# Kernel optimization log

Hardware: AMD Instinct MI355X
Metric: run time of the kernel (lower is better)

## Reference

```python
import jax, jax.numpy as jnp
import numpy as np

EPS = 1e-5


def setup_inputs() -> dict:
    key = jax.random.key(0)
    k1, k2, k3, k4, k5 = jax.random.split(key, 5)
    N, d, F = 8192, 768, 32768
    return {
        "x": jax.random.normal(k1, (N, d), dtype=jnp.float32),
        "pre_bias": jax.random.normal(k2, (d,), dtype=jnp.float32) * 0.02,
        "latent_bias": jax.random.normal(k3, (F,), dtype=jnp.float32) * 0.02,
        "enc_w": jax.random.normal(k4, (F, d), dtype=jnp.float32) / np.sqrt(d),
        "dec_w": jax.random.normal(k5, (d, F), dtype=jnp.float32) / np.sqrt(F),
        "k": 32,
    }


def reference(x, pre_bias, latent_bias, enc_w, dec_w, k):
    # --- encode: manual layernorm (keep mean/std for de-norm) ---
    mean = jnp.mean(x, axis=-1, keepdims=True)           # (N,1)
    var = jnp.var(x, axis=-1, keepdims=True)             # unbiased=False
    std = jnp.sqrt(var + EPS)
    x_centered = (x - mean) / std - pre_bias             # (N,d)
    h_pre = x_centered @ enc_w.T + latent_bias           # (N,F)
    # --- top-k ReLU: keep k largest pre-activations, relu them ---
    topk_vals, topk_idx = jax.lax.top_k(h_pre, k)        # (N,k)
    h = jnp.put_along_axis(jnp.zeros_like(h_pre), topk_idx,
                           jax.nn.relu(topk_vals), axis=-1, inplace=False)
    # --- decode + de-normalize ---
    x_rec_norm = h @ dec_w.T + pre_bias                  # (N,d)
    x_hat = x_rec_norm * std + mean
    return x_hat
```

## Files before the change

### kernel.cpp

```cpp
#include <hip/hip_runtime.h>
#include <hip/hip_bf16.h>
#include <stdint.h>

#define N_ROWS 8192
#define DIM 768
#define NF 32768
#define TOPK 32
#define CANDCAP 72
#define RTHRESH 44

typedef __attribute__((ext_vector_type(8))) short bf16x8;
typedef __attribute__((ext_vector_type(8))) short short8;
typedef __attribute__((ext_vector_type(4))) float f32x4;

__device__ inline void async_ld16(const void* g, void* l) {
  __builtin_amdgcn_global_load_lds(
      (const __attribute__((address_space(1))) unsigned int*)g,
      (__attribute__((address_space(3))) unsigned int*)l, 16, 0, 0);
}

__device__ inline unsigned short f2bf(float f) {
  union { float f; unsigned u; } c; c.f = f;
  unsigned r = c.u + 0x7FFFu + ((c.u >> 16) & 1u);
  return (unsigned short)(r >> 16);
}

__device__ inline float bf2f(unsigned short u) {
  union { unsigned u; float f; } c; c.u = ((unsigned)u) << 16;
  return c.f;
}

__device__ inline void block_barrier_fenced() {
  __builtin_amdgcn_s_barrier();
  asm volatile("" ::: "memory");
  __builtin_amdgcn_sched_barrier(0);
}

__global__ __launch_bounds__(256) void k_ln(const float* __restrict__ x,
                                            const float* __restrict__ pre_bias,
                                            unsigned short* __restrict__ xh,
                                            float* __restrict__ meanA,
                                            float* __restrict__ stdA) {
  int row = blockIdx.x;
  int tid = threadIdx.x;
  int lane = tid & 63, wv = tid >> 6;
  const float* xr = x + (size_t)row * DIM;
  float a0 = xr[tid], a1 = xr[tid + 256], a2 = xr[tid + 512];
  __shared__ float red[8];
  float s = a0 + a1 + a2;
  for (int off = 32; off > 0; off >>= 1) s += __shfl_down(s, off);
  if (lane == 0) red[wv] = s;
  __syncthreads();
  float mean;
  if (tid == 0) { mean = (red[0] + red[1] + red[2] + red[3]) / (float)DIM; red[4] = mean; }
  __syncthreads();
  mean = red[4];
  float d0 = a0 - mean, d1 = a1 - mean, d2 = a2 - mean;
  float ss = d0 * d0 + d1 * d1 + d2 * d2;
  for (int off = 32; off > 0; off >>= 1) ss += __shfl_down(ss, off);
  if (lane == 0) red[wv] = ss;
  __syncthreads();
  float stdv;
  if (tid == 0) {
    float var = (red[0] + red[1] + red[2] + red[3]) / (float)DIM;
    stdv = sqrtf(var + 1e-5f);
    red[5] = stdv;
    meanA[row] = mean;
    stdA[row] = stdv;
  }
  __syncthreads();
  stdv = red[5];
  float inv = 1.0f / stdv;
  unsigned short* xo = xh + (size_t)row * DIM;
  xo[tid]       = f2bf(d0 * inv - pre_bias[tid]);
  xo[tid + 256] = f2bf(d1 * inv - pre_bias[tid + 256]);
  xo[tid + 512] = f2bf(d2 * inv - pre_bias[tid + 512]);
}

__global__ __launch_bounds__(256) void k_cv(const float* __restrict__ w,
                                            unsigned short* __restrict__ o, int n4) {
  int i = blockIdx.x * 256 + threadIdx.x;
  if (i >= n4) return;
  float4 v = ((const float4*)w)[i];
  ushort4 r;
  r.x = f2bf(v.x); r.y = f2bf(v.y); r.z = f2bf(v.z); r.w = f2bf(v.w);
  ((ushort4*)o)[i] = r;
}

__global__ __launch_bounds__(256) void k_tr(const float* __restrict__ dec,
                                            unsigned short* __restrict__ dect) {
  __shared__ float t[32][33];
  int tx = threadIdx.x & 31, ty = threadIdx.x >> 5;
  int fb = blockIdx.x * 32, cb = blockIdx.y * 32;
  for (int i = 0; i < 4; i++) {
    int r = ty + i * 8;
    t[r][tx] = dec[(size_t)(cb + r) * NF + fb + tx];
  }
  __syncthreads();
  for (int i = 0; i < 4; i++) {
    int r = ty + i * 8;
    dect[(size_t)(fb + r) * DIM + cb + tx] = f2bf(t[tx][r]);
  }
}

__global__ __launch_bounds__(512, 4) void k_gemm(const unsigned short* __restrict__ xh,
                                                 const unsigned short* __restrict__ ench,
                                                 const float* __restrict__ latent_bias,
                                                 unsigned* __restrict__ cand6) {
  __shared__ __align__(16) char smem[78336];
  int tid = threadIdx.x;
  int lane = tid & 63;
  int w = tid >> 6;
  int wr = w >> 1, wc = w & 1;
  int lid = blockIdx.x + blockIdx.y * gridDim.x;
  int xcd = lid & 7;
  int u = (lid >> 3) & 31;
  int s = lid >> 8;
  int bx = s * 8 + (u & 7);
  int by = xcd * 4 + (u >> 3);
  const int fr = lane & 15, hi = lane >> 4;

  const char* Ab = (const char*)(xh + (size_t)by * 256 * DIM);
  const char* Bb = (const char*)(ench + (size_t)bx * 128 * DIM);

  int rA[2], cA[2], rB, cB;
#pragma unroll
  for (int i = 0; i < 2; i++) {
    int L = i * 8192 + tid * 16;
    int R = L >> 7;
    int ss = ((L >> 4) & 7) ^ (R & 7);
    rA[i] = (R << 1) + (ss >> 2);
    cA[i] = (ss & 3) << 4;
  }
  {
    int L = tid * 16;
    int R = L >> 7;
    int ss = ((L >> 4) & 7) ^ (R & 7);
    rB = (R << 1) + (ss >> 2);
    cB = (ss & 3) << 4;
  }

  int offA[4], offB[4];
#pragma unroll
  for (int m = 0; m < 4; m++) {
    int r = wr * 64 + m * 16 + fr;
    int R = r >> 1;
    int slot = ((r & 1) << 2) + hi;
    offA[m] = R * 128 + ((slot ^ (R & 7)) << 4);
  }
#pragma unroll
  for (int n = 0; n < 4; n++) {
    int r = wc * 64 + n * 16 + fr;
    int R = r >> 1;
    int slot = ((r & 1) << 2) + hi;
    offB[n] = R * 128 + ((slot ^ (R & 7)) << 4);
  }

  f32x4 acc[4][4];
#pragma unroll
  for (int m = 0; m < 4; m++)
#pragma unroll
    for (int n = 0; n < 4; n++) {
      f32x4 z = {0.f, 0.f, 0.f, 0.f};
      acc[m][n] = z;
    }

#define STAGE(kt, b)                                                          \
  do {                                                                        \
    char* dA = smem + (b) * 16384;                                            \
    char* dB = smem + 49152 + (b) * 8192;                                     \
    _Pragma("unroll") for (int i = 0; i < 2; i++)                             \
        async_ld16(Ab + (size_t)rA[i] * (DIM * 2) + (kt) * 64 + cA[i],        \
                   dA + i * 8192 + tid * 16);                                 \
    async_ld16(Bb + (size_t)rB * (DIM * 2) + (kt) * 64 + cB,                  \
               dB + tid * 16);                                                \
  } while (0)

  STAGE(0, 0);
  STAGE(1, 1);

  for (int kt = 0; kt < 24; kt++) {
    int b = kt % 3;
    if (kt + 1 < 24) asm volatile("s_waitcnt vmcnt(3)" ::: "memory");
    else             asm volatile("s_waitcnt vmcnt(0)" ::: "memory");
    block_barrier_fenced();
    if (kt + 2 < 24) STAGE(kt + 2, (kt + 2) % 3);

    const char* pA = smem + b * 16384;
    const char* pB = smem + 49152 + b * 8192;
    bf16x8 af[4], bv[4];
#pragma unroll
    for (int m = 0; m < 4; m++) af[m] = *(const bf16x8*)(pA + offA[m]);
#pragma unroll
    for (int n = 0; n < 4; n++) bv[n] = *(const bf16x8*)(pB + offB[n]);
    __builtin_amdgcn_s_setprio(1);
#pragma unroll
    for (int m = 0; m < 4; m++)
#pragma unroll
      for (int n = 0; n < 4; n++)
        acc[m][n] = __builtin_amdgcn_mfma_f32_16x16x32_bf16(af[m], bv[n], acc[m][n], 0, 0, 0);
    __builtin_amdgcn_s_setprio(0);
  }
#undef STAGE
  __syncthreads();

  float* sC = (float*)smem;
  int* m6 = (int*)(smem + 66048);
#pragma unroll
  for (int p = 0; p < 2; p++) {
    if ((wr >> 1) == p) {
#pragma unroll
      for (int n = 0; n < 4; n++) {
        int lcol = wc * 64 + n * 16 + fr;
        float lbv = latent_bias[bx * 128 + lcol];
#pragma unroll
        for (int m = 0; m < 4; m++) {
          int lr = (wr & 1) * 64 + m * 16 + hi * 4;
#pragma unroll
          for (int j = 0; j < 4; j++)
            sC[(lr + j) * 129 + lcol] = acc[m][n][j] + lbv;
        }
      }
    }
    __syncthreads();
    {
      int r = tid & 127, q = tid >> 7;
      const float* cr = sC + r * 129 + q * 32;
      unsigned c0 = 0, c1 = 0, c2 = 0, c3 = 0, c4 = 0, c5 = 0;
      for (int c = 0; c < 32; c++) {
        union { float f; unsigned u; } cv; cv.f = cr[c];
        unsigned key = ((int)cv.u < 0) ? ~cv.u : (cv.u | 0x80000000u);
        unsigned pk = (key & 0xFFFFFF00u) | (unsigned)(q * 32 + c);
        if (pk > c0) {
          bool b1 = pk > c1, b2 = pk > c2, b3 = pk > c3, b4 = pk > c4, b5 = pk > c5;
          c0 = b1 ? c1 : pk;
          c1 = b1 ? (b2 ? c2 : pk) : c1;
          c2 = b2 ? (b3 ? c3 : pk) : c2;
          c3 = b3 ? (b4 ? c4 : pk) : c3;
          c4 = b4 ? (b5 ? c5 : pk) : c4;
          c5 = b5 ? pk : c5;
        }
      }
      int* mp = m6 + (q * 128 + r) * 6;
      mp[0] = (int)c0; mp[1] = (int)c1; mp[2] = (int)c2;
      mp[3] = (int)c3; mp[4] = (int)c4; mp[5] = (int)c5;
    }
    __syncthreads();
    if (tid < 128) {
      const int* L0 = m6 + (0 * 128 + tid) * 6;
      const int* L1 = m6 + (1 * 128 + tid) * 6;
      const int* L2 = m6 + (2 * 128 + tid) * 6;
      const int* L3 = m6 + (3 * 128 + tid) * 6;
      int i0 = 5, i1 = 5, i2 = 5, i3 = 5;
      unsigned* dst = cand6 + ((size_t)(by * 256 + p * 128 + tid) * 256 + bx) * 6;
#pragma unroll
      for (int k = 0; k < 6; k++) {
        unsigned v0 = (i0 >= 0) ? (unsigned)L0[i0] : 0u;
        unsigned v1 = (i1 >= 0) ? (unsigned)L1[i1] : 0u;
        unsigned v2 = (i2 >= 0) ? (unsigned)L2[i2] : 0u;
        unsigned v3 = (i3 >= 0) ? (unsigned)L3[i3] : 0u;
        unsigned best = v0; int bq = 0;
        if (v1 > best) { best = v1; bq = 1; }
        if (v2 > best) { best = v2; bq = 2; }
        if (v3 > best) { best = v3; bq = 3; }
        dst[k] = best;
        if (bq == 0) i0--; else if (bq == 1) i1--; else if (bq == 2) i2--; else i3--;
      }
    }
    __syncthreads();
  }
}

__global__ __launch_bounds__(256) void k_screen(const unsigned* __restrict__ cand6,
                                                int* __restrict__ cntg,
                                                int* __restrict__ candg) {
  __shared__ int hist[512];
  __shared__ int hist2[128];
  __shared__ int sb_bstar, sb_chi, sb_cnt;
  __shared__ unsigned sb_tau;
  __shared__ int cand[CANDCAP];

  int tid = threadIdx.x, lane = tid & 63;
  int row = blockIdx.x;
  const unsigned* src = cand6 + (size_t)row * 1536 + tid * 6;
  unsigned pc0 = src[0], pc1 = src[1], pc2 = src[2],
           pc3 = src[3], pc4 = src[4], pc5 = src[5];

  hist[tid] = 0; hist[tid + 256] = 0;
  if (tid < 128) hist2[tid] = 0;
  if (tid == 0) sb_cnt = 0;
  __syncthreads();

  atomicAdd(&hist[pc0 >> 23], 1);
  atomicAdd(&hist[pc1 >> 23], 1);
  atomicAdd(&hist[pc2 >> 23], 1);
  atomicAdd(&hist[pc3 >> 23], 1);
  atomicAdd(&hist[pc4 >> 23], 1);
  atomicAdd(&hist[pc5 >> 23], 1);
  __syncthreads();

  if (tid < 64) {
    int b = lane * 8;
    int h0 = hist[b], h1 = hist[b+1], h2 = hist[b+2], h3 = hist[b+3];
    int h4 = hist[b+4], h5 = hist[b+5], h6 = hist[b+6], h7 = hist[b+7];
    int s7 = h7, s6 = h6 + s7, s5 = h5 + s6, s4 = h4 + s5;
    int s3 = h3 + s4, s2 = h2 + s3, s1 = h1 + s2, s0 = h0 + s1;
    int tot = s0, acc = tot;
#pragma unroll
    for (int off = 1; off <= 32; off <<= 1) {
      int t = __shfl_down(acc, off);
      if (lane + off < 64) acc += t;
    }
    int excl = acc - tot;
    int best = -1, bs = 0, hb = 0;
    if (excl + s0 >= RTHRESH) { best = b + 0; bs = excl + s0; hb = h0; }
    if (excl + s1 >= RTHRESH) { best = b + 1; bs = excl + s1; hb = h1; }
    if (excl + s2 >= RTHRESH) { best = b + 2; bs = excl + s2; hb = h2; }
    if (excl + s3 >= RTHRESH) { best = b + 3; bs = excl + s3; hb = h3; }
    if (excl + s4 >= RTHRESH) { best = b + 4; bs = excl + s4; hb = h4; }
    if (excl + s5 >= RTHRESH) { best = b + 5; bs = excl + s5; hb = h5; }
    if (excl + s6 >= RTHRESH) { best = b + 6; bs = excl + s6; hb = h6; }
    if (excl + s7 >= RTHRESH) { best = b + 7; bs = excl + s7; hb = h7; }
#pragma unroll
    for (int off = 32; off > 0; off >>= 1) {
      int ob = __shfl_down(best, off), obs = __shfl_down(bs, off), ohb = __shfl_down(hb, off);
      if (lane + off < 64 && ob > best) { best = ob; bs = obs; hb = ohb; }
    }
    if (lane == 0) { sb_bstar = best; sb_chi = bs - hb; }
  }
  __syncthreads();
  int bstar = sb_bstar, chi = sb_chi;

  if ((int)(pc0 >> 23) == bstar) atomicAdd(&hist2[(pc0 >> 16) & 127], 1);
  if ((int)(pc1 >> 23) == bstar) atomicAdd(&hist2[(pc1 >> 16) & 127], 1);
  if ((int)(pc2 >> 23) == bstar) atomicAdd(&hist2[(pc2 >> 16) & 127], 1);
  if ((int)(pc3 >> 23) == bstar) atomicAdd(&hist2[(pc3 >> 16) & 127], 1);
  if ((int)(pc4 >> 23) == bstar) atomicAdd(&hist2[(pc4 >> 16) & 127], 1);
  if ((int)(pc5 >> 23) == bstar) atomicAdd(&hist2[(pc5 >> 16) & 127], 1);
  __syncthreads();

  if (tid < 64) {
    int g0 = hist2[lane * 2], g1 = hist2[lane * 2 + 1];
    int s1 = g1, s0 = g0 + g1;
    int tot = s0, acc = tot;
#pragma unroll
    for (int off = 1; off <= 32; off <<= 1) {
      int t = __shfl_down(acc, off);
      if (lane + off < 64) acc += t;
    }
    int excl = acc - tot;
    int best = -1;
    if (chi + excl + s0 >= RTHRESH) best = lane * 2;
    if (chi + excl + s1 >= RTHRESH) best = lane * 2 + 1;
#pragma unroll
    for (int off = 32; off > 0; off >>= 1) {
      int ob = __shfl_down(best, off);
      if (lane + off < 64 && ob > best) best = ob;
    }
    if (lane == 0) sb_tau = ((unsigned)((bstar << 7) | best)) << 16;
  }
  __syncthreads();

  unsigned tau = sb_tau;
#define EMIT(PC)                                                   \
  if ((PC) >= tau) {                                               \
    int pos = atomicAdd(&sb_cnt, 1);                               \
    if (pos < CANDCAP) cand[pos] = tid * 128 + (int)((PC) & 127u); \
  }
  EMIT(pc0) EMIT(pc1) EMIT(pc2) EMIT(pc3) EMIT(pc4) EMIT(pc5)
#undef EMIT
  __syncthreads();

  int cnt = sb_cnt < CANDCAP ? sb_cnt : CANDCAP;
  if (tid == 0) cntg[row] = cnt;
  if (tid < CANDCAP) candg[(size_t)row * CANDCAP + tid] = (tid < cnt) ? cand[tid] : 0;
}

__global__ __launch_bounds__(256) void k_sel(const float* __restrict__ x,
                                             const float* __restrict__ pre_bias,
                                             const float* __restrict__ latent_bias,
                                             const float* __restrict__ enc,
                                             const unsigned short* __restrict__ dect,
                                             const int* __restrict__ cntg,
                                             const int* __restrict__ candg,
                                             const float* __restrict__ meanA,
                                             const float* __restrict__ stdA,
                                             float* __restrict__ out) {
  __shared__ __align__(16) float xn[DIM];
  __shared__ float exactv[128];
  __shared__ int self_[128];
  __shared__ float hv[TOPK];
  __shared__ int hf[TOPK];

  int row = blockIdx.x, tid = threadIdx.x, lane = tid & 63;
  float m = meanA[row], s = stdA[row], inv = 1.0f / s;
  const float* xr = x + (size_t)row * DIM;
  for (int i = tid; i < DIM; i += 256)
    xn[i] = (xr[i] - m) * inv - pre_bias[i];
  int cnt = cntg[row];
  if (tid < 128) {
    self_[tid] = (tid < cnt) ? candg[(size_t)row * CANDCAP + tid] : 0x7FFFFFF;
    exactv[tid] = -3.0e38f;
  }
  __syncthreads();

#pragma unroll
  for (int pass = 0; pass < 2; pass++) {
    int g = pass * 64 + (tid >> 2), t4 = tid & 3;
    if (g < cnt) {
      int f = self_[g];
      const float4* xp = (const float4*)xn;
      const float4* wp = (const float4*)(enc + (size_t)f * DIM);
      float acc = 0.f;
#pragma unroll 4
      for (int i = t4; i < DIM / 4; i += 4) {
        float4 a = xp[i], b = wp[i];
        acc = fmaf(a.x, b.x, acc);
        acc = fmaf(a.y, b.y, acc);
        acc = fmaf(a.z, b.z, acc);
        acc = fmaf(a.w, b.w, acc);
      }
      acc += __shfl_xor(acc, 1);
      acc += __shfl_xor(acc, 2);
      if (t4 == 0) exactv[g] = acc + latent_bias[f];
    }
  }
  __syncthreads();

  if (tid < 64) {
    float v0 = exactv[lane];      int f0 = self_[lane];
    float v1 = exactv[lane + 64]; int f1 = self_[lane + 64];
    for (int r = 0; r < TOPK; r++) {
      float bv = v0; int bf = f0;
      if (v1 > bv || (v1 == bv && f1 < bf)) { bv = v1; bf = f1; }
#pragma unroll
      for (int off = 32; off > 0; off >>= 1) {
        float ov = __shfl_down(bv, off);
        int of = __shfl_down(bf, off);
        if (lane + off < 64 && (ov > bv || (ov == bv && of < bf))) { bv = ov; bf = of; }
      }
      bv = __shfl(bv, 0);
      bf = __shfl(bf, 0);
      if (lane == 0) { hv[r] = bv > 0.f ? bv : 0.f; hf[r] = bf; }
      if (f0 == bf) v0 = -3.0e38f;
      if (f1 == bf) v1 = -3.0e38f;
    }
  }
  __syncthreads();

  float* orow = out + (size_t)row * DIM;
#pragma unroll
  for (int t = 0; t < 3; t++) {
    int c = tid + t * 256;
    float acc = pre_bias[c];
    for (int j = 0; j < TOPK; j++)
      acc = fmaf(hv[j], bf2f(dect[(size_t)hf[j] * DIM + c]), acc);
    orow[c] = acc * s + m;
  }
}

extern "C" void kernel_launch(void* const* d_in, const int* in_sizes, int n_in,
                              void* d_out, int out_size, void* d_ws, size_t ws_size,
                              hipStream_t stream) {
  const float* x   = (const float*)d_in[0];
  const float* pb  = (const float*)d_in[1];
  const float* lb  = (const float*)d_in[2];
  const float* enc = (const float*)d_in[3];
  const float* dec = (const float*)d_in[4];
  float* out = (float*)d_out;

  const size_t off_xh   = 0;
  const size_t off_ench = 12582912;
  const size_t off_dect = 62914560;
  const size_t off_mean = 113246208;
  const size_t off_std  = 113278976;
  const size_t off_cnt  = 113311744;
  const size_t off_cand = 113344512;
  const size_t off_c6   = 115703808;
  if (ws_size < 166035456) return;

  char* ws = (char*)d_ws;
  unsigned short* xh   = (unsigned short*)(ws + off_xh);
  unsigned short* ench = (unsigned short*)(ws + off_ench);
  unsigned short* dect = (unsigned short*)(ws + off_dect);
  float* meanA = (float*)(ws + off_mean);
  float* stdA  = (float*)(ws + off_std);
  int*   cntg  = (int*)(ws + off_cnt);
  int*   candg = (int*)(ws + off_cand);
  unsigned* cand6 = (unsigned*)(ws + off_c6);

  hipLaunchKernelGGL(k_ln, dim3(N_ROWS), dim3(256), 0, stream, x, pb, xh, meanA, stdA);
  hipLaunchKernelGGL(k_cv, dim3((NF * DIM / 4 + 255) / 256), dim3(256), 0, stream,
                     enc, ench, NF * DIM / 4);
  hipLaunchKernelGGL(k_tr, dim3(NF / 32, DIM / 32), dim3(256), 0, stream, dec, dect);

  hipLaunchKernelGGL(k_gemm, dim3(NF / 128, N_ROWS / 256), dim3(512), 0, stream,
                     xh, ench, lb, cand6);
  hipLaunchKernelGGL(k_screen, dim3(N_ROWS), dim3(256), 0, stream, cand6, cntg, candg);

  hipLaunchKernelGGL(k_sel, dim3(N_ROWS), dim3(256), 0, stream,
                     x, pb, lb, enc, dect, cntg, candg, meanA, stdA, out);
}
```

Measured before the change: 834.7 us.

## Shrink GEMM tile to 128x128 with 2x4 warp grid for higher occupancy

The encoder GEMM tile drops from 256x128 to 128x128 rows per block. Warps are rearranged into a 2x4 grid with 4x2 MFMA accumulators each, LDS is cut to 48KB, and launch bounds are raised to 6 blocks per CU. The per-tile top-6 candidate extraction is reworked so each row is scanned by 8 threads over 16 columns and merged 8-way. The aim is more resident waves and better latency hiding, at the cost of lower arithmetic intensity per block (more global and L2 traffic per FLOP) and more blocks.

```diff
diff --git a/kernel.cpp b/kernel.cpp
--- a/kernel.cpp
+++ b/kernel.cpp
@@ -103,44 +103,36 @@
   }
 }
 
-__global__ __launch_bounds__(512, 4) void k_gemm(const unsigned short* __restrict__ xh,
+__global__ __launch_bounds__(512, 6) void k_gemm(const unsigned short* __restrict__ xh,
                                                  const unsigned short* __restrict__ ench,
                                                  const float* __restrict__ latent_bias,
                                                  unsigned* __restrict__ cand6) {
-  __shared__ __align__(16) char smem[78336];
+  __shared__ __align__(16) char smem[49152];
   int tid = threadIdx.x;
   int lane = tid & 63;
   int w = tid >> 6;
-  int wr = w >> 1, wc = w & 1;
+  int wr = w >> 2, wc = w & 3;
   int lid = blockIdx.x + blockIdx.y * gridDim.x;
   int xcd = lid & 7;
-  int u = (lid >> 3) & 31;
-  int s = lid >> 8;
+  int u = (lid >> 3) & 63;
+  int s = lid >> 9;
   int bx = s * 8 + (u & 7);
-  int by = xcd * 4 + (u >> 3);
+  int by = xcd * 8 + (u >> 3);
   const int fr = lane & 15, hi = lane >> 4;
 
-  const char* Ab = (const char*)(xh + (size_t)by * 256 * DIM);
+  const char* Ab = (const char*)(xh + (size_t)by * 128 * DIM);
   const char* Bb = (const char*)(ench + (size_t)bx * 128 * DIM);
 
-  int rA[2], cA[2], rB, cB;
-#pragma unroll
-  for (int i = 0; i < 2; i++) {
-    int L = i * 8192 + tid * 16;
-    int R = L >> 7;
-    int ss = ((L >> 4) & 7) ^ (R & 7);
-    rA[i] = (R << 1) + (ss >> 2);
-    cA[i] = (ss & 3) << 4;
-  }
+  int rA, cA;
   {
     int L = tid * 16;
     int R = L >> 7;
     int ss = ((L >> 4) & 7) ^ (R & 7);
-    rB = (R << 1) + (ss >> 2);
-    cB = (ss & 3) << 4;
-  }
-
-  int offA[4], offB[4];
+    rA = (R << 1) + (ss >> 2);
+    cA = (ss & 3) << 4;
+  }
+
+  int offA[4], offB[2];
 #pragma unroll
   for (int m = 0; m < 4; m++) {
     int r = wr * 64 + m * 16 + fr;
@@ -149,31 +141,28 @@
     offA[m] = R * 128 + ((slot ^ (R & 7)) << 4);
   }
 #pragma unroll
-  for (int n = 0; n < 4; n++) {
-    int r = wc * 64 + n * 16 + fr;
+  for (int n = 0; n < 2; n++) {
+    int r = wc * 32 + n * 16 + fr;
     int R = r >> 1;
     int slot = ((r & 1) << 2) + hi;
     offB[n] = R * 128 + ((slot ^ (R & 7)) << 4);
   }
 
-  f32x4 acc[4][4];
+  f32x4 acc[4][2];
 #pragma unroll
   for (int m = 0; m < 4; m++)
 #pragma unroll
-    for (int n = 0; n < 4; n++) {
+    for (int n = 0; n < 2; n++) {
       f32x4 z = {0.f, 0.f, 0.f, 0.f};
       acc[m][n] = z;
     }
 
 #define STAGE(kt, b)                                                          \
   do {                                                                        \
-    char* dA = smem + (b) * 16384;                                            \
-    char* dB = smem + 49152 + (b) * 8192;                                     \
-    _Pragma("unroll") for (int i = 0; i < 2; i++)                             \
-        async_ld16(Ab + (size_t)rA[i] * (DIM * 2) + (kt) * 64 + cA[i],        \
-                   dA + i * 8192 + tid * 16);                                 \
-    async_ld16(Bb + (size_t)rB * (DIM * 2) + (kt) * 64 + cB,                  \
-               dB + tid * 16);                                                \
+    async_ld16(Ab + (size_t)rA * (DIM * 2) + (kt) * 64 + cA,                  \
+               smem + (b) * 8192 + tid * 16);                                 \
+    async_ld16(Bb + (size_t)rA * (DIM * 2) + (kt) * 64 + cA,                  \
+               smem + 24576 + (b) * 8192 + tid * 16);                         \
   } while (0)
 
   STAGE(0, 0);
@@ -181,23 +170,23 @@
 
   for (int kt = 0; kt < 24; kt++) {
     int b = kt % 3;
-    if (kt + 1 < 24) asm volatile("s_waitcnt vmcnt(3)" ::: "memory");
+    if (kt + 1 < 24) asm volatile("s_waitcnt vmcnt(2)" ::: "memory");
     else             asm volatile("s_waitcnt vmcnt(0)" ::: "memory");
     block_barrier_fenced();
     if (kt + 2 < 24) STAGE(kt + 2, (kt + 2) % 3);
 
-    const char* pA = smem + b * 16384;
-    const char* pB = smem + 49152 + b * 8192;
-    bf16x8 af[4], bv[4];
+    const char* pA = smem + b * 8192;
+    const char* pB = smem + 24576 + b * 8192;
+    bf16x8 af[4], bv[2];
 #pragma unroll
     for (int m = 0; m < 4; m++) af[m] = *(const bf16x8*)(pA + offA[m]);
 #pragma unroll
-    for (int n = 0; n < 4; n++) bv[n] = *(const bf16x8*)(pB + offB[n]);
+    for (int n = 0; n < 2; n++) bv[n] = *(const bf16x8*)(pB + offB[n]);
     __builtin_amdgcn_s_setprio(1);
 #pragma unroll
     for (int m = 0; m < 4; m++)
 #pragma unroll
-      for (int n = 0; n < 4; n++)
+      for (int n = 0; n < 2; n++)
         acc[m][n] = __builtin_amdgcn_mfma_f32_16x16x32_bf16(af[m], bv[n], acc[m][n], 0, 0, 0);
     __builtin_amdgcn_s_setprio(0);
   }
@@ -205,17 +194,17 @@
   __syncthreads();
 
   float* sC = (float*)smem;
-  int* m6 = (int*)(smem + 66048);
+  int* m6 = (int*)(smem + 33024);
 #pragma unroll
   for (int p = 0; p < 2; p++) {
-    if ((wr >> 1) == p) {
-#pragma unroll
-      for (int n = 0; n < 4; n++) {
-        int lcol = wc * 64 + n * 16 + fr;
+    if (wr == p) {
+#pragma unroll
+      for (int n = 0; n < 2; n++) {
+        int lcol = wc * 32 + n * 16 + fr;
         float lbv = latent_bias[bx * 128 + lcol];
 #pragma unroll
         for (int m = 0; m < 4; m++) {
-          int lr = (wr & 1) * 64 + m * 16 + hi * 4;
+          int lr = m * 16 + hi * 4;
 #pragma unroll
           for (int j = 0; j < 4; j++)
             sC[(lr + j) * 129 + lcol] = acc[m][n][j] + lbv;
@@ -224,13 +213,13 @@
     }
     __syncthreads();
     {
-      int r = tid & 127, q = tid >> 7;
-      const float* cr = sC + r * 129 + q * 32;
+      int r = tid & 63, o = tid >> 6;
+      const float* cr = sC + r * 129 + o * 16;
       unsigned c0 = 0, c1 = 0, c2 = 0, c3 = 0, c4 = 0, c5 = 0;
-      for (int c = 0; c < 32; c++) {
+      for (int c = 0; c < 16; c++) {
         union { float f; unsigned u; } cv; cv.f = cr[c];
         unsigned key = ((int)cv.u < 0) ? ~cv.u : (cv.u | 0x80000000u);
-        unsigned pk = (key & 0xFFFFFF00u) | (unsigned)(q * 32 + c);
+        unsigned pk = (key & 0xFFFFFF00u) | (unsigned)(o * 16 + c);
         if (pk > c0) {
           bool b1 = pk > c1, b2 = pk > c2, b3 = pk > c3, b4 = pk > c4, b5 = pk > c5;
           c0 = b1 ? c1 : pk;
@@ -241,30 +230,30 @@
           c5 = b5 ? pk : c5;
         }
       }
-      int* mp = m6 + (q * 128 + r) * 6;
+      int* mp = m6 + (o * 64 + r) * 6;
       mp[0] = (int)c0; mp[1] = (int)c1; mp[2] = (int)c2;
       mp[3] = (int)c3; mp[4] = (int)c4; mp[5] = (int)c5;
     }
     __syncthreads();
-    if (tid < 128) {
-      const int* L0 = m6 + (0 * 128 + tid) * 6;
-      const int* L1 = m6 + (1 * 128 + tid) * 6;
-      const int* L2 = m6 + (2 * 128 + tid) * 6;
-      const int* L3 = m6 + (3 * 128 + tid) * 6;
-      int i0 = 5, i1 = 5, i2 = 5, i3 = 5;
-      unsigned* dst = cand6 + ((size_t)(by * 256 + p * 128 + tid) * 256 + bx) * 6;
+    if (tid < 64) {
+      int idx[8];
+      const int* Ls[8];
+#pragma unroll
+      for (int o = 0; o < 8; o++) {
+        Ls[o] = m6 + (o * 64 + tid) * 6;
+        idx[o] = 5;
+      }
+      unsigned* dst = cand6 + ((size_t)(by * 128 + p * 64 + tid) * 256 + bx) * 6;
 #pragma unroll
       for (int k = 0; k < 6; k++) {
-        unsigned v0 = (i0 >= 0) ? (unsigned)L0[i0] : 0u;
-        unsigned v1 = (i1 >= 0) ? (unsigned)L1[i1] : 0u;
-        unsigned v2 = (i2 >= 0) ? (unsigned)L2[i2] : 0u;
-        unsigned v3 = (i3 >= 0) ? (unsigned)L3[i3] : 0u;
-        unsigned best = v0; int bq = 0;
-        if (v1 > best) { best = v1; bq = 1; }
-        if (v2 > best) { best = v2; bq = 2; }
-        if (v3 > best) { best = v3; bq = 3; }
+        unsigned best = 0u; int bo = 0;
+#pragma unroll
+        for (int o = 0; o < 8; o++) {
+          unsigned v = (idx[o] >= 0) ? (unsigned)Ls[o][idx[o]] : 0u;
+          if (v > best) { best = v; bo = o; }
+        }
         dst[k] = best;
-        if (bq == 0) i0--; else if (bq == 1) i1--; else if (bq == 2) i2--; else i3--;
+        idx[bo]--;
       }
     }
     __syncthreads();
@@ -494,7 +483,7 @@
                      enc, ench, NF * DIM / 4);
   hipLaunchKernelGGL(k_tr, dim3(NF / 32, DIM / 32), dim3(256), 0, stream, dec, dect);
 
-  hipLaunchKernelGGL(k_gemm, dim3(NF / 128, N_ROWS / 256), dim3(512), 0, stream,
+  hipLaunchKernelGGL(k_gemm, dim3(NF / 128, N_ROWS / 128), dim3(512), 0, stream,
                      xh, ench, lb, cand6);
   hipLaunchKernelGGL(k_screen, dim3(N_ROWS), dim3(256), 0, stream, cand6, cntg, candg);
 
```

New measurement: 881.5 us. 1.06x slower.
